# Kernel tuning notes

Hardware: AMD Instinct MI355X
Metric: run time of the kernel (lower is better)

The kernel has to match this reference:

```python
import jax, jax.numpy as jnp
import numpy as np

SQRT_2_OVER_PI = 0.7978845608028654
GELU_COEFF = 0.044715

def _gelu_tanh(v):
    inner = SQRT_2_OVER_PI * (v + GELU_COEFF * v * v * v)
    return 0.5 * v * (1.0 + jnp.tanh(inner))

def setup_inputs() -> dict:
    key = jax.random.key(0)
    k1, k2, k3, k4 = jax.random.split(key, 4)
    M, K, N = 16384, 4096, 4096
    x = jax.random.normal(k1, (M, K), dtype=jnp.float32)
    bound_w = np.sqrt(6.0 / K) / np.sqrt(1.0 + 5.0)  # kaiming_uniform a=sqrt(5)
    weight = jax.random.uniform(k2, (K, N), dtype=jnp.float32, minval=-bound_w, maxval=bound_w)
    bound_b = 1.0 / np.sqrt(K)
    bias = jax.random.uniform(k3, (N,), dtype=jnp.float32, minval=-bound_b, maxval=bound_b)
    subtract = jax.random.normal(k4, (N,), dtype=jnp.float32)
    return {"x": x, "weight": weight, "bias": bias, "subtract": subtract}

def reference(x, weight, bias, subtract):
    # mean_n(xW + b - s) = (x . colsum(W) + sum(b) - sum(s)) / N
    N = weight.shape[1]
    c = weight.sum(axis=1)                       # (K,)
    scale = 1.0 / N
    bias_term = (bias.sum() - subtract.sum()) * scale
    row_scalars = _gelu_tanh(x @ c * scale + bias_term)  # (M,)
    return x + row_scalars[:, None]
```

## Files before the change

### kernel.cpp

```cpp
#include <hip/hip_runtime.h>
#include <math.h>

#define K_DIM 4096
#define N_DIM 4096
#define WAVES_PER_BLOCK 4

__global__ void __launch_bounds__(256) colsum_kernel(const float* __restrict__ W,
                                                     const float* __restrict__ bias,
                                                     const float* __restrict__ subtract,
                                                     float* __restrict__ c,
                                                     float* __restrict__ bterm) {
    const int t = threadIdx.x;
    __shared__ float s[4];
    const int wave = t >> 6, lane = t & 63;

    if (blockIdx.x < K_DIM) {
        const int k = blockIdx.x;
        const float4* row = reinterpret_cast<const float4*>(W + (size_t)k * N_DIM);
        float acc = 0.f;
#pragma unroll
        for (int i = 0; i < N_DIM / 4 / 256; ++i) {
            float4 v = row[t + i * 256];
            acc += (v.x + v.y) + (v.z + v.w);
        }
#pragma unroll
        for (int off = 32; off > 0; off >>= 1) acc += __shfl_down(acc, off, 64);
        if (lane == 0) s[wave] = acc;
        __syncthreads();
        if (t == 0) c[k] = (s[0] + s[1]) + (s[2] + s[3]);
    } else {
        float acc = 0.f;
        for (int i = t; i < N_DIM; i += 256) acc += bias[i] - subtract[i];
#pragma unroll
        for (int off = 32; off > 0; off >>= 1) acc += __shfl_down(acc, off, 64);
        if (lane == 0) s[wave] = acc;
        __syncthreads();
        if (t == 0) bterm[0] = ((s[0] + s[1]) + (s[2] + s[3])) * (1.0f / (float)N_DIM);
    }
}

__global__ void __launch_bounds__(256) rowfuse_kernel(const float* __restrict__ x,
                                                      const float* __restrict__ c,
                                                      const float* __restrict__ bterm,
                                                      float* __restrict__ out) {
    const int t = threadIdx.x;
    const int wave = t >> 6, lane = t & 63;
    const size_t m = (size_t)blockIdx.x * WAVES_PER_BLOCK + wave;

    const float4* xr = reinterpret_cast<const float4*>(x + m * (size_t)K_DIM);
    const float4* c4 = reinterpret_cast<const float4*>(c);
    float4*       orow = reinterpret_cast<float4*>(out + m * (size_t)K_DIM);

    float4 xv[16];
    float a0 = 0.f, a1 = 0.f, a2 = 0.f, a3 = 0.f;
#pragma unroll
    for (int i = 0; i < 16; ++i) {
        xv[i] = xr[lane + i * 64];
        float4 cvv = c4[lane + i * 64];
        a0 += xv[i].x * cvv.x;
        a1 += xv[i].y * cvv.y;
        a2 += xv[i].z * cvv.z;
        a3 += xv[i].w * cvv.w;
    }
    float acc = (a0 + a1) + (a2 + a3);
#pragma unroll
    for (int off = 32; off > 0; off >>= 1) acc += __shfl_xor(acc, off, 64);

    float d = acc * (1.0f / (float)N_DIM) + bterm[0];
    float inner = 0.7978845608028654f * (d + 0.044715f * d * d * d);
    float e  = __expf(2.0f * inner);
    float th = 1.0f - 2.0f / (e + 1.0f);
    float g  = 0.5f * d * (1.0f + th);

#pragma unroll
    for (int i = 0; i < 16; ++i) {
        float4 o = xv[i];
        o.x += g; o.y += g; o.z += g; o.w += g;
        orow[lane + i * 64] = o;
    }
}

extern "C" void kernel_launch(void* const* d_in, const int* in_sizes, int n_in,
                              void* d_out, int out_size, void* d_ws, size_t ws_size,
                              hipStream_t stream) {
    const float* x        = (const float*)d_in[0];
    const float* W        = (const float*)d_in[1];
    const float* bias     = (const float*)d_in[2];
    const float* subtract = (const float*)d_in[3];
    float* out = (float*)d_out;

    float* c     = (float*)d_ws;
    float* bterm = c + K_DIM;

    const int M = in_sizes[0] / K_DIM;

    colsum_kernel<<<K_DIM + 1, 256, 0, stream>>>(W, bias, subtract, c, bterm);
    rowfuse_kernel<<<M / WAVES_PER_BLOCK, 256, 0, stream>>>(x, c, bterm, out);
}
```

Measured before the change: 122.9 us.

## Process four rows per wave with double-buffered loads and nontemporal memory ops

Each wave now handles four consecutive rows, prefetching the next row's x into a second register buffer while it reduces, applies GELU and stores the current row. Loads of W and x and stores of out use nontemporal builtins to avoid polluting cache with streamed data. This is meant to raise memory-level parallelism and hide load latency, at the cost of higher register pressure (two 16-element float4 buffers) and four times fewer blocks.

```diff
diff --git a/kernel.cpp b/kernel.cpp
--- a/kernel.cpp
+++ b/kernel.cpp
@@ -3,7 +3,8 @@
 
 #define K_DIM 4096
 #define N_DIM 4096
-#define WAVES_PER_BLOCK 4
+
+typedef float f32x4 __attribute__((ext_vector_type(4)));
 
 __global__ void __launch_bounds__(256) colsum_kernel(const float* __restrict__ W,
                                                      const float* __restrict__ bias,
@@ -16,11 +17,11 @@
 
     if (blockIdx.x < K_DIM) {
         const int k = blockIdx.x;
-        const float4* row = reinterpret_cast<const float4*>(W + (size_t)k * N_DIM);
+        const f32x4* row = reinterpret_cast<const f32x4*>(W + (size_t)k * N_DIM);
         float acc = 0.f;
 #pragma unroll
         for (int i = 0; i < N_DIM / 4 / 256; ++i) {
-            float4 v = row[t + i * 256];
+            f32x4 v = __builtin_nontemporal_load(&row[t + i * 256]);
             acc += (v.x + v.y) + (v.z + v.w);
         }
 #pragma unroll
@@ -39,45 +40,62 @@
     }
 }
 
+
+#define PROCESS(XV, ROFF)                                                        \
+    do {                                                                         \
+        float a0 = 0.f, a1 = 0.f, a2 = 0.f, a3 = 0.f;                            \
+        _Pragma("unroll")                                                        \
+        for (int i = 0; i < 16; ++i) {                                           \
+            f32x4 cvv = c4[lane + i * 64];                                       \
+            a0 += XV[i].x * cvv.x;                                               \
+            a1 += XV[i].y * cvv.y;                                               \
+            a2 += XV[i].z * cvv.z;                                               \
+            a3 += XV[i].w * cvv.w;                                               \
+        }                                                                        \
+        float acc = (a0 + a1) + (a2 + a3);                                       \
+        _Pragma("unroll")                                                        \
+        for (int off = 32; off > 0; off >>= 1) acc += __shfl_xor(acc, off, 64);  \
+        float d = acc * (1.0f / (float)N_DIM) + bt;                              \
+        float inner = 0.7978845608028654f * (d + 0.044715f * d * d * d);         \
+        float e  = __expf(2.0f * inner);                                         \
+        float g  = 0.5f * d * (1.0f + (1.0f - 2.0f / (e + 1.0f)));               \
+        _Pragma("unroll")                                                        \
+        for (int i = 0; i < 16; ++i) {                                           \
+            f32x4 o = XV[i] + g;                                                 \
+            __builtin_nontemporal_store(o, &orow[(size_t)(ROFF) * 1024 + lane + i * 64]); \
+        }                                                                        \
+    } while (0)
+
 __global__ void __launch_bounds__(256) rowfuse_kernel(const float* __restrict__ x,
                                                       const float* __restrict__ c,
                                                       const float* __restrict__ bterm,
                                                       float* __restrict__ out) {
     const int t = threadIdx.x;
     const int wave = t >> 6, lane = t & 63;
-    const size_t m = (size_t)blockIdx.x * WAVES_PER_BLOCK + wave;
+    const size_t w = (size_t)blockIdx.x * 4 + wave;
 
-    const float4* xr = reinterpret_cast<const float4*>(x + m * (size_t)K_DIM);
-    const float4* c4 = reinterpret_cast<const float4*>(c);
-    float4*       orow = reinterpret_cast<float4*>(out + m * (size_t)K_DIM);
+    const f32x4* c4 = reinterpret_cast<const f32x4*>(c);
+    const f32x4* xr = reinterpret_cast<const f32x4*>(x) + w * 4 * (K_DIM / 4);
+    f32x4* orow     = reinterpret_cast<f32x4*>(out)     + w * 4 * (K_DIM / 4);
+    const float bt = bterm[0];
 
-    float4 xv[16];
-    float a0 = 0.f, a1 = 0.f, a2 = 0.f, a3 = 0.f;
+    f32x4 xa[16], xb[16];
 #pragma unroll
-    for (int i = 0; i < 16; ++i) {
-        xv[i] = xr[lane + i * 64];
-        float4 cvv = c4[lane + i * 64];
-        a0 += xv[i].x * cvv.x;
-        a1 += xv[i].y * cvv.y;
-        a2 += xv[i].z * cvv.z;
-        a3 += xv[i].w * cvv.w;
-    }
-    float acc = (a0 + a1) + (a2 + a3);
-#pragma unroll
-    for (int off = 32; off > 0; off >>= 1) acc += __shfl_xor(acc, off, 64);
-
-    float d = acc * (1.0f / (float)N_DIM) + bterm[0];
-    float inner = 0.7978845608028654f * (d + 0.044715f * d * d * d);
-    float e  = __expf(2.0f * inner);
-    float th = 1.0f - 2.0f / (e + 1.0f);
-    float g  = 0.5f * d * (1.0f + th);
+    for (int i = 0; i < 16; ++i) xa[i] = __builtin_nontemporal_load(&xr[lane + i * 64]);
 
 #pragma unroll
-    for (int i = 0; i < 16; ++i) {
-        float4 o = xv[i];
-        o.x += g; o.y += g; o.z += g; o.w += g;
-        orow[lane + i * 64] = o;
-    }
+    for (int i = 0; i < 16; ++i) xb[i] = __builtin_nontemporal_load(&xr[1024 + lane + i * 64]);
+    PROCESS(xa, 0);
+
+#pragma unroll
+    for (int i = 0; i < 16; ++i) xa[i] = __builtin_nontemporal_load(&xr[2048 + lane + i * 64]);
+    PROCESS(xb, 1);
+
+#pragma unroll
+    for (int i = 0; i < 16; ++i) xb[i] = __builtin_nontemporal_load(&xr[3072 + lane + i * 64]);
+    PROCESS(xa, 2);
+
+    PROCESS(xb, 3);
 }
 
 extern "C" void kernel_launch(void* const* d_in, const int* in_sizes, int n_in,
@@ -95,5 +113,5 @@
     const int M = in_sizes[0] / K_DIM;
 
     colsum_kernel<<<K_DIM + 1, 256, 0, stream>>>(W, bias, subtract, c, bterm);
-    rowfuse_kernel<<<M / WAVES_PER_BLOCK, 256, 0, stream>>>(x, c, bterm, out);
+    rowfuse_kernel<<<M / 16, 256, 0, stream>>>(x, c, bterm, out);
 }
```

Result: faster. 114.8 us (-6.6%).
